# Kernel tuning notes

Hardware: AMD Instinct MI355X
Metric: run time of the kernel (lower is better)

The kernel has to match this reference:

```python
import jax, jax.numpy as jnp
import numpy as np
from jax import lax

B = 65536

def _conv(x, w, b):
    y = lax.conv_general_dilated(x, w, (1, 1), 'VALID',
                                 dimension_numbers=('NCHW', 'OIHW', 'NCHW'))
    return y + b[None, :, None, None]

def _maxpool2(x):
    return lax.reduce_window(x, -jnp.inf, lax.max, (1, 1, 2, 2), (1, 1, 2, 2), 'VALID')

def _cnot01(s):  # control wire0, target wire1; s: [B,2,2] indexed [b,q0,q1]
    return jnp.stack([s[:, 0, :], s[:, 1, ::-1]], axis=1)

def _cnot10(s):  # control wire1, target wire0
    return jnp.stack([s[:, :, 0], s[:, ::-1, 1]], axis=2)

def _ry(half_angle):  # RY(2*half_angle) as used in circuit (theta/2 = half_angle)
    c, si = jnp.cos(half_angle), jnp.sin(half_angle)
    return jnp.stack([jnp.stack([c, -si]), jnp.stack([si, c])]).astype(jnp.complex64)

def _apply_w0(s, U):
    return jnp.einsum('ij,bjk->bik', U, s)

def _apply_w1(s, U):
    return jnp.einsum('ij,bkj->bki', U, s)

def _quantum(x2, p):
    # x2: [B,2] float32, p: [8] float32. Batched 2-qubit statevector sim.
    x0, x1 = x2[:, 0], x2[:, 1]
    n = x2.shape[0]
    s = jnp.full((n, 2, 2), 0.5 + 0.0j, dtype=jnp.complex64)  # H|0> x H|0>
    # RZ(2*x0) on wire 0: diag(e^{-i x0}, e^{i x0})
    s = s * jnp.exp(1j * jnp.stack([-x0, x0], axis=1).astype(jnp.complex64))[:, :, None]
    # RZ(2*x1) on wire 1
    s = s * jnp.exp(1j * jnp.stack([-x1, x1], axis=1).astype(jnp.complex64))[:, None, :]
    s = _cnot01(s)
    ang = (jnp.pi - x0) * (jnp.pi - x1)  # RZ(2*ang) on wire 1
    s = s * jnp.exp(1j * jnp.stack([-ang, ang], axis=1).astype(jnp.complex64))[:, None, :]
    s = _cnot01(s)
    s = _apply_w0(s, _ry(p[0])); s = _apply_w1(s, _ry(p[1])); s = _cnot01(s)
    s = _apply_w0(s, _ry(p[2])); s = _apply_w1(s, _ry(p[3])); s = _cnot10(s)
    s = _apply_w0(s, _ry(p[4])); s = _apply_w1(s, _ry(p[5])); s = _cnot01(s)
    s = _apply_w0(s, _ry(p[6])); s = _apply_w1(s, _ry(p[7]))
    z = jnp.array([[1.0, -1.0], [-1.0, 1.0]], dtype=jnp.float32)  # Z0 (x) Z1 signs
    prob = (s.real ** 2 + s.imag ** 2)
    return jnp.sum(prob * z[None], axis=(1, 2))  # [B]

def setup_inputs() -> dict:
    key = jax.random.key(0)
    ks = jax.random.split(key, 12)
    d = {}
    d['x'] = jax.random.normal(ks[0], (B, 1, 28, 28), dtype=jnp.float32)
    d['conv1_w'] = jax.random.normal(ks[1], (2, 1, 5, 5), dtype=jnp.float32) * 0.2
    d['conv1_b'] = jax.random.normal(ks[2], (2,), dtype=jnp.float32) * 0.1
    d['conv2_w'] = jax.random.normal(ks[3], (16, 2, 5, 5), dtype=jnp.float32) * 0.14
    d['conv2_b'] = jax.random.normal(ks[4], (16,), dtype=jnp.float32) * 0.1
    d['fc1_w'] = jax.random.normal(ks[5], (64, 256), dtype=jnp.float32) * 0.0625
    d['fc1_b'] = jax.random.normal(ks[6], (64,), dtype=jnp.float32) * 0.05
    d['fc2_w'] = jax.random.normal(ks[7], (2, 64), dtype=jnp.float32) * 0.125
    d['fc2_b'] = jax.random.normal(ks[8], (2,), dtype=jnp.float32) * 0.05
    d['fc3_w'] = jax.random.normal(ks[9], (1, 1), dtype=jnp.float32)
    d['fc3_b'] = jax.random.normal(ks[10], (1,), dtype=jnp.float32) * 0.05
    d['qnn_params'] = jax.random.uniform(ks[11], (8,), dtype=jnp.float32)
    return d

def reference(x, conv1_w, conv1_b, conv2_w, conv2_b, fc1_w, fc1_b,
              fc2_w, fc2_b, fc3_w, fc3_b, qnn_params):
    h = jax.nn.relu(_conv(x, conv1_w, conv1_b))        # [B,2,24,24]
    h = _maxpool2(h)                                    # [B,2,12,12]
    h = jax.nn.relu(_conv(h, conv2_w, conv2_b))        # [B,16,8,8]
    h = _maxpool2(h)                                    # [B,16,4,4]
    # Dropout2d: identity in eval mode
    h = h.reshape(h.shape[0], -1)                       # [B,256]
    h = jax.nn.relu(h @ fc1_w.T + fc1_b)                # [B,64]
    h = h @ fc2_w.T + fc2_b                             # [B,2]
    q = _quantum(h, qnn_params)[:, None]                # [B,1]
    y = q @ fc3_w.T + fc3_b                             # [B,1]
    logits = jnp.concatenate([y, 1.0 - y], axis=-1)     # [B,2]
    return jax.nn.log_softmax(logits, axis=1)
```

## Files before the change

kernel.cpp:

```cpp
#include <hip/hip_runtime.h>
#include <math.h>


typedef float v2f __attribute__((ext_vector_type(2)));
typedef float f32x4 __attribute__((ext_vector_type(4)));
typedef short bf16x8 __attribute__((ext_vector_type(8)));
typedef unsigned int u32x4 __attribute__((ext_vector_type(4)));

union B8 { unsigned int u[4]; bf16x8 v; };

static __device__ __forceinline__ v2f vmax2(v2f a, v2f b) {
    return __builtin_elementwise_max(a, b);
}

#define PK_FMA_W0(acc, w, xp) \
    asm("v_pk_fma_f32 %0, %1, %2, %0 op_sel:[0,0,0] op_sel_hi:[1,0,1]" \
        : "+v"(acc) : "s"(w), "v"(xp))
#define PK_FMA_W1(acc, w, xp) \
    asm("v_pk_fma_f32 %0, %1, %2, %0 op_sel:[0,1,0] op_sel_hi:[1,1,1]" \
        : "+v"(acc) : "s"(w), "v"(xp))

#define MFMA16(a, b, c) __builtin_amdgcn_mfma_f32_16x16x32_bf16(a, b, c, 0, 0, 0)

#define SEL_HI 0x07060302u
#define SEL_LO 0x05040100u

static __device__ __forceinline__ unsigned int pack1(float v) {
    unsigned int hi = __float_as_uint(v) & 0xFFFF0000u;
    float lo = v - __uint_as_float(hi);
    return hi | (__float_as_uint(lo) >> 16);
}

#define A2_HI 0
#define A2_LO 1536
#define A1_HI 3072
#define A1_LO (3072 + 16384)

#define P1_S 300

__global__ __launch_bounds__(256)
void hqcnn_prep(const float* __restrict__ w2, const float* __restrict__ fw1,
                unsigned short* __restrict__ ws) {
    int t = blockIdx.x * 256 + threadIdx.x;
    if (blockIdx.x == 0) {
        for (int e = threadIdx.x; e < 1536; e += 256) {
            int cc = e >> 9, r = e & 511;
            int lid = r >> 3, j = r & 7;
            int nn = lid & 15, qq = lid >> 4;
            int row = cc * 4 + qq;
            int ch = (row >= 5) ? 1 : 0;
            int u = row - 5 * ch;
            float val = (row < 10 && j < 5) ? w2[nn * 50 + ch * 25 + u * 5 + j] : 0.f;
            unsigned int uu = __float_as_uint(val);
            float lo = val - __uint_as_float(uu & 0xFFFF0000u);
            ws[A2_HI + e] = (unsigned short)(uu >> 16);
            ws[A2_LO + e] = (unsigned short)(__float_as_uint(lo) >> 16);
        }
    }
    for (int e = t; e < 16384; e += gridDim.x * 256) {
        int m = e >> 8, kp = e & 255;
        int oc = kp & 15, s16 = kp >> 4;
        float val = fw1[m * 256 + oc * 16 + s16];
        unsigned int u = __float_as_uint(val);
        float lo = val - __uint_as_float(u & 0xFFFF0000u);
        ws[A1_HI + e] = (unsigned short)(u >> 16);
        ws[A1_LO + e] = (unsigned short)(__float_as_uint(lo) >> 16);
    }
}

__global__ __launch_bounds__(256, 8)
void hqcnn_fused(const float* __restrict__ x,
                 const float* __restrict__ w1,
                 const float* __restrict__ b1,
                 const float* __restrict__ b2,
                 const float* __restrict__ fb1,
                 const float* __restrict__ fw2,
                 const float* __restrict__ fb2,
                 const float* __restrict__ fw3,
                 const float* __restrict__ fb3,
                 const float* __restrict__ qp,
                 const unsigned short* __restrict__ ws,
                 float* __restrict__ out)
{
    __shared__ __align__(16) unsigned int p1u[16 * P1_S];
    __shared__ __align__(16) float zbuf[4 * 32];

    const int t = threadIdx.x;
    const int wv = t >> 6;
    const int lane = t & 63;
    const int n = lane & 15;
    const int q = lane >> 4;
    const long base = (long)blockIdx.x * 16;

    if (t < 128)
        p1u[(t >> 3) * P1_S + 288 + (t & 7)] = 0u;

    {
        v2f w1p[25];
        #pragma unroll
        for (int k = 0; k < 25; ++k)
            w1p[k] = (v2f){w1[k], w1[25 + k]};
        const v2f bias1 = (v2f){b1[0], b1[1]};

        #pragma unroll
        for (int it = 0; it < 3; ++it) {
            int f = t + it * 256;
            int s = f / 48;
            int r = f - s * 48;
            int i = r >> 2, jh = r & 3;
            const float* xrow = x + (base + s) * 784;
            v2f acc[12];
            #pragma unroll
            for (int qq = 0; qq < 12; ++qq) acc[qq] = (v2f){0.f, 0.f};
            #pragma unroll
            for (int u = 0; u < 6; ++u) {
                const v2f* xp = (const v2f*)(xrow + (2 * i + u) * 28 + 6 * jh);
                v2f P[5] = { xp[0], xp[1], xp[2], xp[3], xp[4] };
                #pragma unroll
                for (int a = 0; a < 2; ++a) {
                    if (a <= u && (u - a) <= 4) {
                        const int wu = u - a;
                        #pragma unroll
                        for (int v = 0; v < 5; ++v) {
                            #pragma unroll
                            for (int j = 0; j < 6; ++j) {
                                const int e = j + v;
                                if (e & 1) { PK_FMA_W1(acc[a * 6 + j], w1p[wu * 5 + v], P[e >> 1]); }
                                else       { PK_FMA_W0(acc[a * 6 + j], w1p[wu * 5 + v], P[e >> 1]); }
                            }
                        }
                    }
                }
            }
            #pragma unroll
            for (int m = 0; m < 3; ++m) {
                v2f mx = vmax2(vmax2(acc[2 * m], acc[2 * m + 1]),
                               vmax2(acc[6 + 2 * m], acc[7 + 2 * m]));
                mx = mx + bias1;
                mx = vmax2(mx, (v2f){0.f, 0.f});
                int pc = 3 * jh + m;
                int off = s * P1_S + i * 12 + pc;
                p1u[off] = pack1(mx.x);
                p1u[off + 144] = pack1(mx.y);
            }
        }
    }
    __syncthreads();

    {
        const bf16x8* B2h = (const bf16x8*)(ws + A2_HI);
        const bf16x8* B2l = (const bf16x8*)(ws + A2_LO);
        bf16x8 b_h[3], b_l[3];
        #pragma unroll
        for (int cc = 0; cc < 3; ++cc) {
            b_h[cc] = B2h[cc * 64 + lane];
            b_l[cc] = B2l[cc * 64 + lane];
        }
        const int quad = n >> 2;
        const int di = (n >> 1) & 1;
        const int dj = n & 1;
        const int scol = 2 * quad + dj;
        int chu[3];
        #pragma unroll
        for (int cc = 0; cc < 3; ++cc) {
            int row = cc * 4 + q;
            int ch = (row >= 5) ? 1 : 0;
            int u = row - 5 * ch;
            chu[cc] = (row < 10) ? (ch * 144 + u * 12) : -1;
        }
        const float bias = b2[n];

        for (int sp = 0; sp < 4; ++sp) {
            const int smp = 4 * wv + sp;
            const int sbase = smp * P1_S;
            const int zaddr = sbase + 288;
            float pvv[4];
            #pragma unroll
            for (int tt = 0; tt < 4; ++tt) {
                int pbase = sbase + (2 * tt + di) * 12 + scol;
                f32x4 acc = {0.f, 0.f, 0.f, 0.f};
                f32x4 acc2 = {0.f, 0.f, 0.f, 0.f};
                #pragma unroll
                for (int cc = 0; cc < 3; ++cc) {
                    int a = (chu[cc] >= 0) ? (pbase + chu[cc]) : zaddr;
                    unsigned int e0 = p1u[a],     e1 = p1u[a + 1], e2 = p1u[a + 2],
                                 e3 = p1u[a + 3], e4 = p1u[a + 4];
                    B8 AH, AL;
                    AH.u[0] = __builtin_amdgcn_perm(e1, e0, SEL_HI);
                    AH.u[1] = __builtin_amdgcn_perm(e3, e2, SEL_HI);
                    AH.u[2] = e4 >> 16;
                    AH.u[3] = 0u;
                    AL.u[0] = __builtin_amdgcn_perm(e1, e0, SEL_LO);
                    AL.u[1] = __builtin_amdgcn_perm(e3, e2, SEL_LO);
                    AL.u[2] = e4 & 0xFFFFu;
                    AL.u[3] = 0u;
                    acc  = MFMA16(AH.v, b_h[cc], acc);
                    acc2 = MFMA16(AL.v, b_h[cc], acc2);
                    acc  = MFMA16(AH.v, b_l[cc], acc);
                }
                acc = acc + acc2;
                float pv = fmaxf(fmaxf(acc[0], acc[1]), fmaxf(acc[2], acc[3]));
                pvv[tt] = fmaxf(pv + bias, 0.f);
            }
            #pragma unroll
            for (int tt = 0; tt < 4; ++tt)
                p1u[sbase + tt * 64 + lane] = pack1(pvv[tt]);
        }
    }
    __syncthreads();

    {
        const bf16x8* A1h = (const bf16x8*)(ws + A1_HI);
        const bf16x8* A1l = (const bf16x8*)(ws + A1_LO);
        const int abase = (wv * 16 + n) * 32 + q;
        f32x4 acc = {0.f, 0.f, 0.f, 0.f};
        f32x4 acc2 = {0.f, 0.f, 0.f, 0.f};
        #pragma unroll
        for (int kk = 0; kk < 8; ++kk) {
            bf16x8 ah = A1h[abase + kk * 4];
            bf16x8 al = A1l[abase + kk * 4];
            const u32x4* hp = (const u32x4*)(p1u + n * P1_S + kk * 32 + q * 8);
            u32x4 d0 = hp[0], d1 = hp[1];
            B8 BH, BL;
            BH.u[0] = __builtin_amdgcn_perm(d0.y, d0.x, SEL_HI);
            BH.u[1] = __builtin_amdgcn_perm(d0.w, d0.z, SEL_HI);
            BH.u[2] = __builtin_amdgcn_perm(d1.y, d1.x, SEL_HI);
            BH.u[3] = __builtin_amdgcn_perm(d1.w, d1.z, SEL_HI);
            BL.u[0] = __builtin_amdgcn_perm(d0.y, d0.x, SEL_LO);
            BL.u[1] = __builtin_amdgcn_perm(d0.w, d0.z, SEL_LO);
            BL.u[2] = __builtin_amdgcn_perm(d1.y, d1.x, SEL_LO);
            BL.u[3] = __builtin_amdgcn_perm(d1.w, d1.z, SEL_LO);
            acc  = MFMA16(ah, BH.v, acc);
            acc2 = MFMA16(ah, BL.v, acc2);
            acc  = MFMA16(al, BH.v, acc);
        }
        acc = acc + acc2;
        f32x4 fb4 = *(const f32x4*)(fb1 + wv * 16 + q * 4);
        f32x4 w20 = *(const f32x4*)(fw2 + wv * 16 + q * 4);
        f32x4 w21 = *(const f32x4*)(fw2 + 64 + wv * 16 + q * 4);
        float p0 = 0.f, p1v = 0.f;
        #pragma unroll
        for (int r = 0; r < 4; ++r) {
            float a = fmaxf(acc[r] + fb4[r], 0.f);
            p0  = fmaf(a, w20[r], p0);
            p1v = fmaf(a, w21[r], p1v);
        }
        p0  += __shfl_xor(p0, 16, 64);  p0  += __shfl_xor(p0, 32, 64);
        p1v += __shfl_xor(p1v, 16, 64); p1v += __shfl_xor(p1v, 32, 64);
        if (q == 0) {
            zbuf[wv * 32 + n * 2]     = p0;
            zbuf[wv * 32 + n * 2 + 1] = p1v;
        }
    }
    __syncthreads();
    if (wv != 0) return;

    {
        int s = lane & 15;
        float x0 = fb2[0] + zbuf[s * 2]     + zbuf[32 + s * 2]
                          + zbuf[64 + s * 2] + zbuf[96 + s * 2];
        float x1 = fb2[1] + zbuf[s * 2 + 1] + zbuf[32 + s * 2 + 1]
                          + zbuf[64 + s * 2 + 1] + zbuf[96 + s * 2 + 1];

        float sr[4], si[4];
        {
            float th0 = -x0 - x1, th1 = -x0 + x1, th2 = x0 - x1, th3 = x0 + x1;
            sr[0] = 0.5f * __cosf(th0); si[0] = 0.5f * __sinf(th0);
            sr[1] = 0.5f * __cosf(th1); si[1] = 0.5f * __sinf(th1);
            sr[2] = 0.5f * __cosf(th2); si[2] = 0.5f * __sinf(th2);
            sr[3] = 0.5f * __cosf(th3); si[3] = 0.5f * __sinf(th3);
        }
        {
            float tr = sr[2]; sr[2] = sr[3]; sr[3] = tr;
            float ti = si[2]; si[2] = si[3]; si[3] = ti;
            float ang = ((float)M_PI - x0) * ((float)M_PI - x1);
            float ca = __cosf(ang), sa = __sinf(ang);
            float r, im;
            r = sr[0]; im = si[0]; sr[0] = r*ca + im*sa; si[0] = im*ca - r*sa;
            r = sr[2]; im = si[2]; sr[2] = r*ca + im*sa; si[2] = im*ca - r*sa;
            r = sr[1]; im = si[1]; sr[1] = r*ca - im*sa; si[1] = im*ca + r*sa;
            r = sr[3]; im = si[3]; sr[3] = r*ca - im*sa; si[3] = im*ca + r*sa;
            tr = sr[2]; sr[2] = sr[3]; sr[3] = tr;
            ti = si[2]; si[2] = si[3]; si[3] = ti;
        }
        float cp[8], sp[8];
        #pragma unroll
        for (int g = 0; g < 8; ++g) { float qv = qp[g]; cp[g] = __cosf(qv); sp[g] = __sinf(qv); }

        #define QRY0(cc, ss) { \
            float a0r=sr[0], a0i=si[0], a1r=sr[2], a1i=si[2]; \
            sr[0]=cc*a0r-ss*a1r; si[0]=cc*a0i-ss*a1i; \
            sr[2]=ss*a0r+cc*a1r; si[2]=ss*a0i+cc*a1i; \
            float b0r=sr[1], b0i=si[1], b1r=sr[3], b1i=si[3]; \
            sr[1]=cc*b0r-ss*b1r; si[1]=cc*b0i-ss*b1i; \
            sr[3]=ss*b0r+cc*b1r; si[3]=ss*b0i+cc*b1i; }
        #define QRY1(cc, ss) { \
            float a0r=sr[0], a0i=si[0], a1r=sr[1], a1i=si[1]; \
            sr[0]=cc*a0r-ss*a1r; si[0]=cc*a0i-ss*a1i; \
            sr[1]=ss*a0r+cc*a1r; si[1]=ss*a0i+cc*a1i; \
            float b0r=sr[2], b0i=si[2], b1r=sr[3], b1i=si[3]; \
            sr[2]=cc*b0r-ss*b1r; si[2]=cc*b0i-ss*b1i; \
            sr[3]=ss*b0r+cc*b1r; si[3]=ss*b0i+cc*b1i; }
        #define QSWAP(i_, j_) { float tr=sr[i_]; sr[i_]=sr[j_]; sr[j_]=tr; \
                                float ti=si[i_]; si[i_]=si[j_]; si[j_]=ti; }

        QRY0(cp[0], sp[0]);
        QRY1(cp[1], sp[1]);
        QSWAP(2, 3);
        QRY0(cp[2], sp[2]);
        QRY1(cp[3], sp[3]);
        QSWAP(1, 3);
        QRY0(cp[4], sp[4]);
        QRY1(cp[5], sp[5]);
        QSWAP(2, 3);
        QRY0(cp[6], sp[6]);
        QRY1(cp[7], sp[7]);

        float qv = (sr[0]*sr[0] + si[0]*si[0])
                 - (sr[1]*sr[1] + si[1]*si[1])
                 - (sr[2]*sr[2] + si[2]*si[2])
                 + (sr[3]*sr[3] + si[3]*si[3]);
        float y = fmaf(qv, fw3[0], fb3[0]);
        float l0 = y, l1 = 1.0f - y;
        float m = fmaxf(l0, l1);
        float lse = m + __logf(__expf(l0 - m) + __expf(l1 - m));
        if (lane < 32) {
            int comp = lane >> 4;
            out[(base + s) * 2 + comp] = comp ? (l1 - lse) : (l0 - lse);
        }
        #undef QRY0
        #undef QRY1
        #undef QSWAP
    }
}

extern "C" void kernel_launch(void* const* d_in, const int* in_sizes, int n_in,
                              void* d_out, int out_size, void* d_ws, size_t ws_size,
                              hipStream_t stream) {
    const float* x   = (const float*)d_in[0];
    const float* w1  = (const float*)d_in[1];
    const float* b1  = (const float*)d_in[2];
    const float* w2  = (const float*)d_in[3];
    const float* b2  = (const float*)d_in[4];
    const float* fw1 = (const float*)d_in[5];
    const float* fb1 = (const float*)d_in[6];
    const float* fw2 = (const float*)d_in[7];
    const float* fb2 = (const float*)d_in[8];
    const float* fw3 = (const float*)d_in[9];
    const float* fb3 = (const float*)d_in[10];
    const float* qp  = (const float*)d_in[11];
    float* outp = (float*)d_out;
    unsigned short* wsp = (unsigned short*)d_ws;

    hipLaunchKernelGGL(hqcnn_prep, dim3(64), dim3(256), 0, stream, w2, fw1, wsp);

    int B = in_sizes[0] / 784;
    int nblk = B / 16;
    hipLaunchKernelGGL(hqcnn_fused, dim3(nblk), dim3(256), 0, stream,
                       x, w1, b1, b2, fb1, fw2, fb2, fw3, fb3, qp, wsp, outp);
}
```

Baseline: 370.8 us.

## Make conv1 work wave-local and drop the block barrier before conv2

```diff
diff --git a/kernel.cpp b/kernel.cpp
--- a/kernel.cpp
+++ b/kernel.cpp
@@ -92,8 +92,8 @@
     const int q = lane >> 4;
     const long base = (long)blockIdx.x * 16;
 
-    if (t < 128)
-        p1u[(t >> 3) * P1_S + 288 + (t & 7)] = 0u;
+    if (lane < 32)
+        p1u[(4 * wv + (lane >> 3)) * P1_S + 288 + (lane & 7)] = 0u;
 
     {
         v2f w1p[25];
@@ -104,18 +104,28 @@
 
         #pragma unroll
         for (int it = 0; it < 3; ++it) {
-            int f = t + it * 256;
-            int s = f / 48;
-            int r = f - s * 48;
+            int idx = it * 64 + lane;
+            int sl = idx / 48;
+            int r = idx - sl * 48;
             int i = r >> 2, jh = r & 3;
-            const float* xrow = x + (base + s) * 784;
+            const int s = 4 * wv + sl;
+            const float* xrow = x + (base + s) * 784 + 6 * jh;
             v2f acc[12];
             #pragma unroll
             for (int qq = 0; qq < 12; ++qq) acc[qq] = (v2f){0.f, 0.f};
+            v2f P[2][5];
+            {
+                const v2f* xp = (const v2f*)(xrow + (2 * i) * 28);
+                #pragma unroll
+                for (int v5 = 0; v5 < 5; ++v5) P[0][v5] = xp[v5];
+            }
             #pragma unroll
             for (int u = 0; u < 6; ++u) {
-                const v2f* xp = (const v2f*)(xrow + (2 * i + u) * 28 + 6 * jh);
-                v2f P[5] = { xp[0], xp[1], xp[2], xp[3], xp[4] };
+                if (u < 5) {
+                    const v2f* xp = (const v2f*)(xrow + (2 * i + u + 1) * 28);
+                    #pragma unroll
+                    for (int v5 = 0; v5 < 5; ++v5) P[(u + 1) & 1][v5] = xp[v5];
+                }
                 #pragma unroll
                 for (int a = 0; a < 2; ++a) {
                     if (a <= u && (u - a) <= 4) {
@@ -125,8 +135,8 @@
                             #pragma unroll
                             for (int j = 0; j < 6; ++j) {
                                 const int e = j + v;
-                                if (e & 1) { PK_FMA_W1(acc[a * 6 + j], w1p[wu * 5 + v], P[e >> 1]); }
-                                else       { PK_FMA_W0(acc[a * 6 + j], w1p[wu * 5 + v], P[e >> 1]); }
+                                if (e & 1) { PK_FMA_W1(acc[a * 6 + j], w1p[wu * 5 + v], P[u & 1][e >> 1]); }
+                                else       { PK_FMA_W0(acc[a * 6 + j], w1p[wu * 5 + v], P[u & 1][e >> 1]); }
                             }
                         }
                     }
@@ -145,7 +155,7 @@
             }
         }
     }
-    __syncthreads();
+    asm volatile("s_waitcnt lgkmcnt(0)" ::: "memory");
 
     {
         const bf16x8* B2h = (const bf16x8*)(ws + A2_HI);
@@ -175,6 +185,7 @@
             const int sbase = smp * P1_S;
             const int zaddr = sbase + 288;
             float pvv[4];
+            __builtin_amdgcn_s_setprio(1);
             #pragma unroll
             for (int tt = 0; tt < 4; ++tt) {
                 int pbase = sbase + (2 * tt + di) * 12 + scol;
@@ -202,6 +213,7 @@
                 float pv = fmaxf(fmaxf(acc[0], acc[1]), fmaxf(acc[2], acc[3]));
                 pvv[tt] = fmaxf(pv + bias, 0.f);
             }
+            __builtin_amdgcn_s_setprio(0);
             #pragma unroll
             for (int tt = 0; tt < 4; ++tt)
                 p1u[sbase + tt * 64 + lane] = pack1(pvv[tt]);
@@ -215,6 +227,7 @@
         const int abase = (wv * 16 + n) * 32 + q;
         f32x4 acc = {0.f, 0.f, 0.f, 0.f};
         f32x4 acc2 = {0.f, 0.f, 0.f, 0.f};
+        __builtin_amdgcn_s_setprio(1);
         #pragma unroll
         for (int kk = 0; kk < 8; ++kk) {
             bf16x8 ah = A1h[abase + kk * 4];
@@ -234,6 +247,7 @@
             acc2 = MFMA16(ah, BL.v, acc2);
             acc  = MFMA16(al, BH.v, acc);
         }
+        __builtin_amdgcn_s_setprio(0);
         acc = acc + acc2;
         f32x4 fb4 = *(const f32x4*)(fb1 + wv * 16 + q * 4);
         f32x4 w20 = *(const f32x4*)(fw2 + wv * 16 + q * 4);
```

After: 404.0 us. 1.09x slower.
